# Kernel optimization log

Hardware: AMD Instinct MI355X
Metric: run time of the kernel (lower is better)

## Reference

```python
import jax, jax.numpy as jnp
import numpy as np

DIM = 1024
B, L = 8, 2048
ACT = DIM // 4          # sparse_ratio 0.25
HID = DIM // 4          # LowRankFF reduction 4
EPS = 1e-6
K, DILATION = 5, 1
PAD = (K - 1) * DILATION // 2


def setup_inputs() -> dict:
    key = jax.random.key(0)
    ks = jax.random.split(key, 16)
    s = lambda fan_in: 1.0 / np.sqrt(fan_in)
    return {
        "x": jax.random.normal(ks[0], (B, L, DIM), jnp.float32),
        "norm_w": jnp.ones((DIM,), jnp.float32),
        "dw_w": jax.random.normal(ks[1], (DIM, 1, K), jnp.float32) * s(K),
        "dw_b": jax.random.normal(ks[2], (DIM,), jnp.float32) * s(K),
        "pw_w": jax.random.normal(ks[3], (DIM, DIM), jnp.float32) * s(DIM),
        "pw_b": jax.random.normal(ks[4], (DIM,), jnp.float32) * s(DIM),
        "alpha": jnp.full((ACT,), 0.9, jnp.float32),
        "beta": jnp.full((ACT,), 0.1, jnp.float32),
        "W1_w": jax.random.normal(ks[5], (DIM, DIM), jnp.float32) * s(DIM),
        "W1_b": jax.random.normal(ks[6], (DIM,), jnp.float32) * s(DIM),
        "W2_w": jax.random.normal(ks[7], (DIM, DIM), jnp.float32) * s(DIM),
        "W2_b": jax.random.normal(ks[8], (DIM,), jnp.float32) * s(DIM),
        "down_w": jax.random.normal(ks[9], (HID, DIM), jnp.float32) * s(DIM),
        "down_b": jax.random.normal(ks[10], (HID,), jnp.float32) * s(DIM),
        "up_w": jax.random.normal(ks[11], (DIM, HID), jnp.float32) * s(HID),
        "up_b": jax.random.normal(ks[12], (DIM,), jnpp := jnp.float32) * s(HID),
    }


def reference(x, norm_w, dw_w, dw_b, pw_w, pw_b, alpha, beta,
              W1_w, W1_b, W2_w, W2_b, down_w, down_b, up_w, up_b):
    residual = x
    # RMSNorm
    rms = jnp.sqrt(jnp.mean(x * x, axis=-1, keepdims=True) + EPS)
    xn = norm_w * (x / rms)                              # [B,L,D]
    # depthwise conv (groups=DIM), NCH layout; same-length output
    xc = jax.lax.conv_general_dilated(
        xn.transpose(0, 2, 1), dw_w,
        window_strides=(1,), padding=[(PAD, PAD)],
        rhs_dilation=(DILATION,), feature_group_count=DIM,
        dimension_numbers=("NCH", "OIH", "NCH")) + dw_b[None, :, None]
    xc = xc.transpose(0, 2, 1)                           # [B,L,D]
    # pointwise conv == dense linear over channels
    x_conv = jnp.einsum("bld,od->blo", xc, pw_w) + pw_b
    # sparse shift-gate recurrence on FIRST ACT channels (faithful to source)
    x_act = xn[:, :, :ACT]                               # [B,L,A]

    def step(h, xt):                                     # h,xt: [B,A]
        h = alpha * h + beta * xt
        return h, h

    _, hs = jax.lax.scan(step, jnp.zeros((B, ACT), xn.dtype),
                         x_act.transpose(1, 0, 2))       # hs: [L,B,A]
    x_rec = jnp.concatenate([hs.transpose(1, 0, 2), xn[:, :, ACT:]], axis=-1)
    # gated fusion
    y = x_conv + x_rec
    y = y + jax.nn.sigmoid(y @ W1_w.T + W1_b) * jnp.tanh(y @ W2_w.T + W2_b)
    # low-rank FF (exact gelu, matching torch F.gelu default)
    y = y + (jax.nn.gelu(y @ down_w.T + down_b, approximate=False) @ up_w.T + up_b)
    return y + residual
```

## Files before the change

kernel.cpp:

```cpp
#include <hip/hip_runtime.h>
#include <math.h>

#define DIMC 1024
#define BB   8
#define LL   2048
#define ACTC 256
#define HIDC 256
#define EPSV 1e-6f
#define MROWS (BB * LL)
#define NCHUNK 32
#define LC     64

typedef __bf16 bf16x8 __attribute__((ext_vector_type(8)));
typedef float  f32x4  __attribute__((ext_vector_type(4)));

__device__ __forceinline__ unsigned short f2bf(float f) {
    union { float f; unsigned int u; } v; v.f = f;
    unsigned int u = v.u + 0x7fffu + ((v.u >> 16) & 1u);
    return (unsigned short)(u >> 16);
}
__device__ __forceinline__ float bf2f(unsigned short s) {
    union { float f; unsigned int u; } v; v.u = ((unsigned int)s) << 16;
    return v.f;
}
__device__ __forceinline__ float fast_sigmoid(float x) {
    return 1.0f / (1.0f + __expf(-x));
}
__device__ __forceinline__ float fast_tanh(float x) {
    float ax = fabsf(x);
    float t = 1.0f - 2.0f / (__expf(2.0f * ax) + 1.0f);
    return copysignf(t, x);
}

__global__ void k_convert5(const float* __restrict__ s0, const float* __restrict__ s1,
                           const float* __restrict__ s2, const float* __restrict__ s3,
                           const float* __restrict__ s4,
                           unsigned short* __restrict__ d0, unsigned short* __restrict__ d12,
                           unsigned short* __restrict__ d3, unsigned short* __restrict__ d4) {
    int i = blockIdx.x * blockDim.x + threadIdx.x;
    if (i < 1048576) {
        d0[i] = f2bf(s0[i]);
    } else if (i < 2097152) {
        int j = i - 1048576; int n = j >> 10, kk = j & 1023;
        d12[(size_t)(n * 2) * 1024 + kk] = f2bf(s1[j]);
    } else if (i < 3145728) {
        int j = i - 2097152; int n = j >> 10, kk = j & 1023;
        d12[(size_t)(n * 2 + 1) * 1024 + kk] = f2bf(s2[j]);
    } else if (i < 3407872) {
        d3[i - 3145728] = f2bf(s3[i - 3145728]);
    } else if (i < 3670016) {
        d4[i - 3407872] = f2bf(s4[i - 3407872]);
    }
}

__global__ __launch_bounds__(256, 2) void k_normconv(
        const float* __restrict__ x, const float* __restrict__ w,
        const float* __restrict__ dww, const float* __restrict__ dwb,
        unsigned short* __restrict__ xnb, unsigned short* __restrict__ xc) {
    __shared__ unsigned short sxn[36 * 1024];
    int blk = blockIdx.x;
    int b = blk >> 6, s = blk & 63;
    int l0 = s * 32;
    int t = threadIdx.x;
    int lane = t & 63, wid = t >> 6;

    float4 nw[4];
#pragma unroll
    for (int j = 0; j < 4; ++j) nw[j] = ((const float4*)w)[j * 64 + lane];

    for (int rr = wid; rr < 36; rr += 4) {
        int l = l0 - 2 + rr;
        bool inr = (l >= 0 && l < LL);
        float4 v[4];
#pragma unroll
        for (int j = 0; j < 4; ++j) { v[j].x = 0.f; v[j].y = 0.f; v[j].z = 0.f; v[j].w = 0.f; }
        if (inr) {
            const float4* xp = (const float4*)(x + ((size_t)b * LL + l) * DIMC);
#pragma unroll
            for (int j = 0; j < 4; ++j) v[j] = xp[j * 64 + lane];
        }
        float ss = 0.f;
#pragma unroll
        for (int j = 0; j < 4; ++j)
            ss += v[j].x * v[j].x + v[j].y * v[j].y + v[j].z * v[j].z + v[j].w * v[j].w;
#pragma unroll
        for (int off = 1; off < 64; off <<= 1) ss += __shfl_xor(ss, off, 64);
        float rinv = 1.0f / sqrtf(ss * (1.0f / DIMC) + EPSV);
#pragma unroll
        for (int j = 0; j < 4; ++j) {
            uint2 o;
            o.x = (unsigned)f2bf(nw[j].x * v[j].x * rinv) | ((unsigned)f2bf(nw[j].y * v[j].y * rinv) << 16);
            o.y = (unsigned)f2bf(nw[j].z * v[j].z * rinv) | ((unsigned)f2bf(nw[j].w * v[j].w * rinv) << 16);
            ((uint2*)(sxn + rr * 1024))[j * 64 + lane] = o;
            if (inr && rr >= 2 && rr < 34)
                ((uint2*)(xnb + ((size_t)b * LL + l) * DIMC))[j * 64 + lane] = o;
        }
    }
    __syncthreads();

    float wgt[4][5];
    int c0 = t * 4;
#pragma unroll
    for (int j = 0; j < 4; ++j)
#pragma unroll
        for (int k = 0; k < 5; ++k) wgt[j][k] = dww[(c0 + j) * 5 + k];
    float4 bv = ((const float4*)dwb)[t];
    for (int r = 0; r < 32; ++r) {
        float acc[4] = {bv.x, bv.y, bv.z, bv.w};
#pragma unroll
        for (int k = 0; k < 5; ++k) {
            uint2 rv = ((const uint2*)(sxn + (r + k) * 1024))[t];
            acc[0] += bf2f((unsigned short)(rv.x & 0xffff)) * wgt[0][k];
            acc[1] += bf2f((unsigned short)(rv.x >> 16))    * wgt[1][k];
            acc[2] += bf2f((unsigned short)(rv.y & 0xffff)) * wgt[2][k];
            acc[3] += bf2f((unsigned short)(rv.y >> 16))    * wgt[3][k];
        }
        uint2 o;
        o.x = (unsigned)f2bf(acc[0]) | ((unsigned)f2bf(acc[1]) << 16);
        o.y = (unsigned)f2bf(acc[2]) | ((unsigned)f2bf(acc[3]) << 16);
        ((uint2*)(xc + ((size_t)b * LL + l0 + r) * DIMC))[t] = o;
    }
}

__global__ __launch_bounds__(256) void k_scan_a(const unsigned short* __restrict__ xnb,
                                                const float* __restrict__ alpha,
                                                const float* __restrict__ beta,
                                                float* __restrict__ F) {
    int blk = blockIdx.x;
    int b = blk >> 5, k = blk & (NCHUNK - 1);
    int c = threadIdx.x;
    float a = alpha[c], bt = beta[c];
    const unsigned short* p = xnb + ((size_t)(b * LL + k * LC)) * DIMC + c;
    float h = 0.0f;
    for (int l = 0; l < LC; ++l) h = a * h + bt * bf2f(p[(size_t)l * DIMC]);
    F[(size_t)blk * ACTC + c] = h;
}
__global__ __launch_bounds__(256) void k_scan_c(const unsigned short* __restrict__ xnb,
                                                const float* __restrict__ alpha,
                                                const float* __restrict__ beta,
                                                const float* __restrict__ F,
                                                unsigned short* __restrict__ hs) {
    int blk = blockIdx.x;
    int b = blk >> 5, k = blk & (NCHUNK - 1);
    int c = threadIdx.x;
    float a = alpha[c], bt = beta[c];
    float aL = a;
#pragma unroll
    for (int i = 0; i < 6; ++i) aL *= aL;
    float T = 0.0f;
    for (int j = 0; j < k; ++j)
        T = F[((size_t)b * NCHUNK + j) * ACTC + c] + aL * T;
    const unsigned short* p = xnb + ((size_t)(b * LL + k * LC)) * DIMC + c;
    unsigned short*       q = hs  + ((size_t)(b * LL + k * LC)) * ACTC + c;
    float h = T;
    for (int l = 0; l < LC; ++l) {
        h = a * h + bt * bf2f(p[(size_t)l * DIMC]);
        q[(size_t)l * ACTC] = f2bf(h);
    }
}

#define TM 128
#define TN 128
#define BK 64

#define GLOAD_LDS(gp, lp) \
    __builtin_amdgcn_global_load_lds((const __attribute__((address_space(1))) unsigned int*)(gp), \
                                     (__attribute__((address_space(3))) unsigned int*)(lp), 16, 0, 0)

template<int MODE>
__global__ __launch_bounds__(256, 4) void k_gemm(
        const unsigned short* __restrict__ A,
        const unsigned short* __restrict__ B0,
        const float* __restrict__ bias0,
        const float* __restrict__ bias1,
        const unsigned short* __restrict__ add0,
        const unsigned short* __restrict__ add1,
        const float* __restrict__ addf,
        float* __restrict__ outf,
        unsigned short* __restrict__ outb,
        int M, int N, int K)
{
    __shared__ __align__(16) char lds[32768];
    unsigned short* sA  = (unsigned short*)lds;
    unsigned short* sB0 = (unsigned short*)(lds + 16384);

    int nx = gridDim.x;
    int bid = blockIdx.y * nx + blockIdx.x;
    int xcd = bid & 7, s = bid >> 3;
    int colt = s % nx, rowgrp = s / nx;
    int m0 = (rowgrp * 8 + xcd) * TM;
    int n0 = colt * TN;

    int t = threadIdx.x;
    int w = t >> 6, lane = t & 63;
    int wm = (w >> 1) * 64, wn = (w & 1) * 64;
    int quad = lane >> 4, lm = lane & 15;
    int lm7 = lm & 7;

    f32x4 zero = {0.f, 0.f, 0.f, 0.f};
    f32x4 acc0[4][4];
#pragma unroll
    for (int i = 0; i < 4; ++i)
#pragma unroll
        for (int j = 0; j < 4; ++j) acc0[i][j] = zero;

    for (int k0 = 0; k0 < K; k0 += BK) {
        __syncthreads();
#pragma unroll
        for (int c = 0; c < 4; ++c) {
            int i = t + c * 256;
            int r = i >> 3;
            int sc = ((i & 7) ^ (r & 7)) << 3;
            GLOAD_LDS(A  + (size_t)(m0 + r) * K + k0 + sc, sA  + i * 8);
            GLOAD_LDS(B0 + (size_t)(n0 + r) * K + k0 + sc, sB0 + i * 8);
        }
        __syncthreads();

#pragma unroll
        for (int ks = 0; ks < BK; ks += 32) {
            int cgb = ks >> 3;
            bf16x8 af[4], b0f[4];
#pragma unroll
            for (int i = 0; i < 4; ++i) {
                int sg = ((cgb + quad) ^ lm7) << 3;
                af[i]  = *(const bf16x8*)(sA  + (wm + i * 16 + lm) * BK + sg);
                b0f[i] = *(const bf16x8*)(sB0 + (wn + i * 16 + lm) * BK + sg);
            }
#pragma unroll
            for (int mi = 0; mi < 4; ++mi)
#pragma unroll
                for (int ni = 0; ni < 4; ++ni)
                    acc0[mi][ni] = __builtin_amdgcn_mfma_f32_16x16x32_bf16(af[mi], b0f[ni], acc0[mi][ni], 0, 0, 0);
        }
    }

    __syncthreads();
    if constexpr (MODE == 3) {
        float* sO = (float*)lds;
#pragma unroll
        for (int half = 0; half < 2; ++half) {
            if (wm == half * 64) {
#pragma unroll
                for (int mi = 0; mi < 4; ++mi) {
#pragma unroll
                    for (int ni = 0; ni < 4; ++ni) {
                        int nl = wn + ni * 16 + lm;
                        float bn = bias0[n0 + nl];
#pragma unroll
                        for (int j = 0; j < 4; ++j) {
                            int mloc = mi * 16 + quad * 4 + j;
                            sO[mloc * TN + nl] = acc0[mi][ni][j] + bn;
                        }
                    }
                }
            }
            __syncthreads();
#pragma unroll
            for (int c = 0; c < 8; ++c) {
                int i = t + c * 256;
                int r = i >> 5, c4 = (i & 31) << 2;
                int m = m0 + half * 64 + r, n = n0 + c4;
                float4 v  = *(float4*)(sO + r * TN + c4);
                uint2  ab = *(const uint2*)(add0 + (size_t)m * N + n);
                float4 xf = *(const float4*)(addf + (size_t)m * N + n);
                float4 o;
                o.x = v.x + bf2f((unsigned short)(ab.x & 0xffff)) + xf.x;
                o.y = v.y + bf2f((unsigned short)(ab.x >> 16))    + xf.y;
                o.z = v.z + bf2f((unsigned short)(ab.y & 0xffff)) + xf.z;
                o.w = v.w + bf2f((unsigned short)(ab.y >> 16))    + xf.w;
                *(float4*)(outf + (size_t)m * N + n) = o;
            }
            __syncthreads();
        }
    } else if constexpr (MODE == 4) {
        unsigned short* sO = (unsigned short*)lds;
#pragma unroll
        for (int mi = 0; mi < 4; ++mi) {
#pragma unroll
            for (int ni = 0; ni < 4; ++ni) {
                int nl = wn + ni * 16 + lm;
                int ng = n0 + nl;
                float bn = (nl & 1) ? bias1[ng >> 1] : bias0[ng >> 1];
#pragma unroll
                for (int j = 0; j < 4; ++j) {
                    int ml = wm + mi * 16 + quad * 4 + j;
                    float u  = acc0[mi][ni][j] + bn;
                    float uo = __shfl_xor(u, 1, 64);
                    float ue = (nl & 1) ? uo : u;
                    float ut = (nl & 1) ? u  : uo;
                    float r = fast_sigmoid(ue) * fast_tanh(ut);
                    if (!(nl & 1)) sO[ml * 64 + (nl >> 1)] = f2bf(r);
                }
            }
        }
        __syncthreads();
#pragma unroll
        for (int c = 0; c < 4; ++c) {
            int i = t + c * 256;
            int r = i >> 3, c8 = (i & 7) << 3;
            int m = m0 + r, n = (n0 >> 1) + c8;
            uint4 g  = *(uint4*)(sO + r * 64 + c8);
            uint4 av = *(const uint4*)(add0 + (size_t)m * DIMC + n);
            unsigned* gp = (unsigned*)&g;
            unsigned* ap = (unsigned*)&av;
            uint4 o; unsigned* op = (unsigned*)&o;
#pragma unroll
            for (int q = 0; q < 4; ++q) {
                float lo = bf2f((unsigned short)(gp[q] & 0xffff)) + bf2f((unsigned short)(ap[q] & 0xffff));
                float hi = bf2f((unsigned short)(gp[q] >> 16))    + bf2f((unsigned short)(ap[q] >> 16));
                op[q] = (unsigned)f2bf(lo) | ((unsigned)f2bf(hi) << 16);
            }
            *(uint4*)(outb + (size_t)m * DIMC + n) = o;
        }
    } else {
        unsigned short* sO = (unsigned short*)lds;
#pragma unroll
        for (int mi = 0; mi < 4; ++mi) {
#pragma unroll
            for (int ni = 0; ni < 4; ++ni) {
                int nl = wn + ni * 16 + lm;
                int n  = n0 + nl;
                float bn = bias0[n];
#pragma unroll
                for (int j = 0; j < 4; ++j) {
                    int ml = wm + mi * 16 + quad * 4 + j;
                    float v = acc0[mi][ni][j];
                    float r;
                    if constexpr (MODE == 0) {
                        r = v + bn;
                    } else {
                        float u = v + bn;
                        r = 0.5f * u * (1.0f + erff(u * 0.70710678118654752f));
                    }
                    sO[ml * TN + nl] = f2bf(r);
                }
            }
        }
        __syncthreads();
#pragma unroll
        for (int c = 0; c < 8; ++c) {
            int i = t + c * 256;
            int r = i >> 4, c8 = (i & 15) << 3;
            int m = m0 + r, n = n0 + c8;
            uint4 g = *(uint4*)(sO + r * TN + c8);
            if constexpr (MODE == 2) {
                *(uint4*)(outb + (size_t)m * N + n) = g;
            } else {
                uint4 av = (n0 < ACTC) ? *(const uint4*)(add0 + (size_t)m * ACTC + n)
                                       : *(const uint4*)(add1 + (size_t)m * DIMC + n);
                unsigned* gp = (unsigned*)&g;
                unsigned* ap = (unsigned*)&av;
                uint4 o;
                unsigned* op = (unsigned*)&o;
#pragma unroll
                for (int q = 0; q < 4; ++q) {
                    float lo = bf2f((unsigned short)(gp[q] & 0xffff)) + bf2f((unsigned short)(ap[q] & 0xffff));
                    float hi = bf2f((unsigned short)(gp[q] >> 16))    + bf2f((unsigned short)(ap[q] >> 16));
                    op[q] = (unsigned)f2bf(lo) | ((unsigned)f2bf(hi) << 16);
                }
                *(uint4*)(outb + (size_t)m * N + n) = o;
            }
        }
    }
}

template<int MODE>
__global__ __launch_bounds__(256, 4) void k_gemm64(
        const unsigned short* __restrict__ A,
        const unsigned short* __restrict__ B0,
        const float* __restrict__ bias0,
        unsigned short* __restrict__ outb,
        int M, int N, int K)
{
    __shared__ __align__(16) char lds[24576];
    unsigned short* sA  = (unsigned short*)lds;
    unsigned short* sB0 = (unsigned short*)(lds + 16384);

    int nx = gridDim.x;
    int bid = blockIdx.y * nx + blockIdx.x;
    int xcd = bid & 7, s = bid >> 3;
    int colt = s % nx, rowgrp = s / nx;
    int m0 = (rowgrp * 8 + xcd) * TM;
    int n0 = colt * 64;

    int t = threadIdx.x;
    int w = t >> 6, lane = t & 63;
    int wm = (w >> 1) * 64, wn = (w & 1) * 32;
    int quad = lane >> 4, lm = lane & 15;
    int lm7 = lm & 7;

    f32x4 zero = {0.f, 0.f, 0.f, 0.f};
    f32x4 acc0[4][2];
#pragma unroll
    for (int i = 0; i < 4; ++i)
#pragma unroll
        for (int j = 0; j < 2; ++j) acc0[i][j] = zero;

    for (int k0 = 0; k0 < K; k0 += BK) {
        __syncthreads();
#pragma unroll
        for (int c = 0; c < 4; ++c) {
            int i = t + c * 256;
            int r = i >> 3;
            int sc = ((i & 7) ^ (r & 7)) << 3;
            GLOAD_LDS(A + (size_t)(m0 + r) * K + k0 + sc, sA + i * 8);
        }
#pragma unroll
        for (int c = 0; c < 2; ++c) {
            int i = t + c * 256;
            int r = i >> 3;
            int sc = ((i & 7) ^ (r & 7)) << 3;
            GLOAD_LDS(B0 + (size_t)(n0 + r) * K + k0 + sc, sB0 + i * 8);
        }
        __syncthreads();

#pragma unroll
        for (int ks = 0; ks < BK; ks += 32) {
            int cgb = ks >> 3;
            int sg = ((cgb + quad) ^ lm7) << 3;
            bf16x8 af[4], b0f[2];
#pragma unroll
            for (int i = 0; i < 4; ++i)
                af[i] = *(const bf16x8*)(sA + (wm + i * 16 + lm) * BK + sg);
#pragma unroll
            for (int i = 0; i < 2; ++i)
                b0f[i] = *(const bf16x8*)(sB0 + (wn + i * 16 + lm) * BK + sg);
#pragma unroll
            for (int mi = 0; mi < 4; ++mi)
#pragma unroll
                for (int ni = 0; ni < 2; ++ni)
                    acc0[mi][ni] = __builtin_amdgcn_mfma_f32_16x16x32_bf16(af[mi], b0f[ni], acc0[mi][ni], 0, 0, 0);
        }
    }

    __syncthreads();
    unsigned short* sO = (unsigned short*)lds;
#pragma unroll
    for (int mi = 0; mi < 4; ++mi) {
#pragma unroll
        for (int ni = 0; ni < 2; ++ni) {
            int nl = wn + ni * 16 + lm;
            int n  = n0 + nl;
            float bn = bias0[n];
#pragma unroll
            for (int j = 0; j < 4; ++j) {
                int ml = wm + mi * 16 + quad * 4 + j;
                float u = acc0[mi][ni][j] + bn;
                float r = 0.5f * u * (1.0f + erff(u * 0.70710678118654752f));
                sO[ml * 64 + nl] = f2bf(r);
            }
        }
    }
    __syncthreads();
#pragma unroll
    for (int c = 0; c < 4; ++c) {
        int i = t + c * 256;
        int r = i >> 3, c8 = (i & 7) << 3;
        int m = m0 + r, n = n0 + c8;
        uint4 g = *(uint4*)(sO + r * 64 + c8);
        *(uint4*)(outb + (size_t)m * N + n) = g;
    }
}

extern "C" void kernel_launch(void* const* d_in, const int* in_sizes, int n_in,
                              void* d_out, int out_size, void* d_ws, size_t ws_size,
                              hipStream_t stream) {
    (void)in_sizes; (void)n_in; (void)out_size; (void)ws_size;
    const float* x      = (const float*)d_in[0];
    const float* norm_w = (const float*)d_in[1];
    const float* dw_w   = (const float*)d_in[2];
    const float* dw_b   = (const float*)d_in[3];
    const float* pw_w   = (const float*)d_in[4];
    const float* pw_b   = (const float*)d_in[5];
    const float* alpha  = (const float*)d_in[6];
    const float* beta   = (const float*)d_in[7];
    const float* W1_w   = (const float*)d_in[8];
    const float* W1_b   = (const float*)d_in[9];
    const float* W2_w   = (const float*)d_in[10];
    const float* W2_b   = (const float*)d_in[11];
    const float* down_w = (const float*)d_in[12];
    const float* down_b = (const float*)d_in[13];
    const float* up_w   = (const float*)d_in[14];
    const float* up_b   = (const float*)d_in[15];

    char* ws = (char*)d_ws;
    unsigned short* xnb  = (unsigned short*)(ws);
    unsigned short* xc   = (unsigned short*)(ws + 33554432ull);
    unsigned short* hs   = (unsigned short*)(ws + 67108864ull);
    unsigned short* y1b  = (unsigned short*)(ws + 75497472ull);
    unsigned short* y2b  = (unsigned short*)(ws + 109051904ull);
    unsigned short* gact = (unsigned short*)(ws + 142606336ull);
    unsigned short* wpw  = (unsigned short*)(ws + 150994944ull);
    unsigned short* w12  = wpw + 1048576;
    unsigned short* wdn  = wpw + 3145728;
    unsigned short* wup  = wdn + 262144;
    float*          Fb   = (float*)(ws + 159383552ull);

    k_convert5<<<14336, 256, 0, stream>>>(pw_w, W1_w, W2_w, down_w, up_w,
                                          wpw, w12, wdn, wup);

    k_normconv<<<BB * 64, 256, 0, stream>>>(x, norm_w, dw_w, dw_b, xnb, xc);

    k_scan_a<<<BB * NCHUNK, ACTC, 0, stream>>>(xnb, alpha, beta, Fb);
    k_scan_c<<<BB * NCHUNK, ACTC, 0, stream>>>(xnb, alpha, beta, Fb, hs);

    dim3 g0(DIMC / TN, MROWS / TM);
    dim3 g1(2 * DIMC / TN, MROWS / TM);
    dim3 g2(HIDC / 64, MROWS / TM);
    k_gemm<0><<<g0, 256, 0, stream>>>(xc, wpw, pw_b, nullptr, hs, xnb, nullptr, nullptr, y1b, MROWS, DIMC, DIMC);
    k_gemm<4><<<g1, 256, 0, stream>>>(y1b, w12, W1_b, W2_b, y1b, nullptr, nullptr, nullptr, y2b, MROWS, 2 * DIMC, DIMC);
    k_gemm64<2><<<g2, 256, 0, stream>>>(y2b, wdn, down_b, gact, MROWS, HIDC, DIMC);
    k_gemm<3><<<g0, 256, 0, stream>>>(gact, wup, up_b, nullptr, y2b, nullptr, x, (float*)d_out, nullptr, MROWS, DIMC, HIDC);
}
```

Measured before the change: 372.6 us.

## Compute W1 and W2 GEMMs in one kernel with dual accumulators sharing A tile

Replaces the interleaved 2048-wide W1/W2 GEMM, which paired sigmoid and tanh columns via lane shuffles, with a dual-B GEMM. Each block loads one A tile and two B tiles and keeps two accumulator sets, then applies sigmoid*tanh directly in the epilogue. This halves the number of A-tile loads and removes the shuffle and the interleaved weight layout. The cost is more registers and LDS per block, so occupancy drops to 2 waves per SIMD.

```diff
diff --git a/kernel.cpp b/kernel.cpp
--- a/kernel.cpp
+++ b/kernel.cpp
@@ -35,22 +35,15 @@
 __global__ void k_convert5(const float* __restrict__ s0, const float* __restrict__ s1,
                            const float* __restrict__ s2, const float* __restrict__ s3,
                            const float* __restrict__ s4,
-                           unsigned short* __restrict__ d0, unsigned short* __restrict__ d12,
-                           unsigned short* __restrict__ d3, unsigned short* __restrict__ d4) {
+                           unsigned short* __restrict__ d0, unsigned short* __restrict__ d1,
+                           unsigned short* __restrict__ d2, unsigned short* __restrict__ d3,
+                           unsigned short* __restrict__ d4) {
     int i = blockIdx.x * blockDim.x + threadIdx.x;
-    if (i < 1048576) {
-        d0[i] = f2bf(s0[i]);
-    } else if (i < 2097152) {
-        int j = i - 1048576; int n = j >> 10, kk = j & 1023;
-        d12[(size_t)(n * 2) * 1024 + kk] = f2bf(s1[j]);
-    } else if (i < 3145728) {
-        int j = i - 2097152; int n = j >> 10, kk = j & 1023;
-        d12[(size_t)(n * 2 + 1) * 1024 + kk] = f2bf(s2[j]);
-    } else if (i < 3407872) {
-        d3[i - 3145728] = f2bf(s3[i - 3145728]);
-    } else if (i < 3670016) {
-        d4[i - 3407872] = f2bf(s4[i - 3407872]);
-    }
+    if (i < 1048576)            d0[i]           = f2bf(s0[i]);
+    else if (i < 2097152)       d1[i - 1048576] = f2bf(s1[i - 1048576]);
+    else if (i < 3145728)       d2[i - 2097152] = f2bf(s2[i - 2097152]);
+    else if (i < 3407872)       d3[i - 3145728] = f2bf(s3[i - 3145728]);
+    else if (i < 3670016)       d4[i - 3407872] = f2bf(s4[i - 3407872]);
 }
 
 __global__ __launch_bounds__(256, 2) void k_normconv(
@@ -168,9 +161,10 @@
                                      (__attribute__((address_space(3))) unsigned int*)(lp), 16, 0, 0)
 
 template<int MODE>
-__global__ __launch_bounds__(256, 4) void k_gemm(
+__device__ __forceinline__ void gemm_body(
         const unsigned short* __restrict__ A,
         const unsigned short* __restrict__ B0,
+        const unsigned short* __restrict__ B1,
         const float* __restrict__ bias0,
         const float* __restrict__ bias1,
         const unsigned short* __restrict__ add0,
@@ -180,9 +174,11 @@
         unsigned short* __restrict__ outb,
         int M, int N, int K)
 {
-    __shared__ __align__(16) char lds[32768];
+    constexpr int LDSB = (MODE == 1) ? 49152 : 32768;
+    __shared__ __align__(16) char lds[LDSB];
     unsigned short* sA  = (unsigned short*)lds;
     unsigned short* sB0 = (unsigned short*)(lds + 16384);
+    unsigned short* sB1 = (unsigned short*)(lds + 32768);
 
     int nx = gridDim.x;
     int bid = blockIdx.y * nx + blockIdx.x;
@@ -199,10 +195,17 @@
 
     f32x4 zero = {0.f, 0.f, 0.f, 0.f};
     f32x4 acc0[4][4];
+    f32x4 acc1[(MODE == 1) ? 4 : 1][(MODE == 1) ? 4 : 1];
 #pragma unroll
     for (int i = 0; i < 4; ++i)
 #pragma unroll
         for (int j = 0; j < 4; ++j) acc0[i][j] = zero;
+    if constexpr (MODE == 1) {
+#pragma unroll
+        for (int i = 0; i < 4; ++i)
+#pragma unroll
+            for (int j = 0; j < 4; ++j) acc1[i][j] = zero;
+    }
 
     for (int k0 = 0; k0 < K; k0 += BK) {
         __syncthreads();
@@ -213,6 +216,8 @@
             int sc = ((i & 7) ^ (r & 7)) << 3;
             GLOAD_LDS(A  + (size_t)(m0 + r) * K + k0 + sc, sA  + i * 8);
             GLOAD_LDS(B0 + (size_t)(n0 + r) * K + k0 + sc, sB0 + i * 8);
+            if constexpr (MODE == 1)
+                GLOAD_LDS(B1 + (size_t)(n0 + r) * K + k0 + sc, sB1 + i * 8);
         }
         __syncthreads();
 
@@ -226,11 +231,25 @@
                 af[i]  = *(const bf16x8*)(sA  + (wm + i * 16 + lm) * BK + sg);
                 b0f[i] = *(const bf16x8*)(sB0 + (wn + i * 16 + lm) * BK + sg);
             }
-#pragma unroll
-            for (int mi = 0; mi < 4; ++mi)
-#pragma unroll
-                for (int ni = 0; ni < 4; ++ni)
-                    acc0[mi][ni] = __builtin_amdgcn_mfma_f32_16x16x32_bf16(af[mi], b0f[ni], acc0[mi][ni], 0, 0, 0);
+            if constexpr (MODE == 1) {
+                bf16x8 b1f[4];
+#pragma unroll
+                for (int i = 0; i < 4; ++i)
+                    b1f[i] = *(const bf16x8*)(sB1 + (wn + i * 16 + lm) * BK + (((cgb + quad) ^ lm7) << 3));
+#pragma unroll
+                for (int mi = 0; mi < 4; ++mi)
+#pragma unroll
+                    for (int ni = 0; ni < 4; ++ni) {
+                        acc0[mi][ni] = __builtin_amdgcn_mfma_f32_16x16x32_bf16(af[mi], b0f[ni], acc0[mi][ni], 0, 0, 0);
+                        acc1[mi][ni] = __builtin_amdgcn_mfma_f32_16x16x32_bf16(af[mi], b1f[ni], acc1[mi][ni], 0, 0, 0);
+                    }
+            } else {
+#pragma unroll
+                for (int mi = 0; mi < 4; ++mi)
+#pragma unroll
+                    for (int ni = 0; ni < 4; ++ni)
+                        acc0[mi][ni] = __builtin_amdgcn_mfma_f32_16x16x32_bf16(af[mi], b0f[ni], acc0[mi][ni], 0, 0, 0);
+            }
         }
     }
 
@@ -272,46 +291,6 @@
             }
             __syncthreads();
         }
-    } else if constexpr (MODE == 4) {
-        unsigned short* sO = (unsigned short*)lds;
-#pragma unroll
-        for (int mi = 0; mi < 4; ++mi) {
-#pragma unroll
-            for (int ni = 0; ni < 4; ++ni) {
-                int nl = wn + ni * 16 + lm;
-                int ng = n0 + nl;
-                float bn = (nl & 1) ? bias1[ng >> 1] : bias0[ng >> 1];
-#pragma unroll
-                for (int j = 0; j < 4; ++j) {
-                    int ml = wm + mi * 16 + quad * 4 + j;
-                    float u  = acc0[mi][ni][j] + bn;
-                    float uo = __shfl_xor(u, 1, 64);
-                    float ue = (nl & 1) ? uo : u;
-                    float ut = (nl & 1) ? u  : uo;
-                    float r = fast_sigmoid(ue) * fast_tanh(ut);
-                    if (!(nl & 1)) sO[ml * 64 + (nl >> 1)] = f2bf(r);
-                }
-            }
-        }
-        __syncthreads();
-#pragma unroll
-        for (int c = 0; c < 4; ++c) {
-            int i = t + c * 256;
-            int r = i >> 3, c8 = (i & 7) << 3;
-            int m = m0 + r, n = (n0 >> 1) + c8;
-            uint4 g  = *(uint4*)(sO + r * 64 + c8);
-            uint4 av = *(const uint4*)(add0 + (size_t)m * DIMC + n);
-            unsigned* gp = (unsigned*)&g;
-            unsigned* ap = (unsigned*)&av;
-            uint4 o; unsigned* op = (unsigned*)&o;
-#pragma unroll
-            for (int q = 0; q < 4; ++q) {
-                float lo = bf2f((unsigned short)(gp[q] & 0xffff)) + bf2f((unsigned short)(ap[q] & 0xffff));
-                float hi = bf2f((unsigned short)(gp[q] >> 16))    + bf2f((unsigned short)(ap[q] >> 16));
-                op[q] = (unsigned)f2bf(lo) | ((unsigned)f2bf(hi) << 16);
-            }
-            *(uint4*)(outb + (size_t)m * DIMC + n) = o;
-        }
     } else {
         unsigned short* sO = (unsigned short*)lds;
 #pragma unroll
@@ -321,6 +300,7 @@
                 int nl = wn + ni * 16 + lm;
                 int n  = n0 + nl;
                 float bn = bias0[n];
+                float bn1 = (MODE == 1) ? bias1[n] : 0.0f;
 #pragma unroll
                 for (int j = 0; j < 4; ++j) {
                     int ml = wm + mi * 16 + quad * 4 + j;
@@ -329,8 +309,9 @@
                     if constexpr (MODE == 0) {
                         r = v + bn;
                     } else {
-                        float u = v + bn;
-                        r = 0.5f * u * (1.0f + erff(u * 0.70710678118654752f));
+                        float u1 = v + bn;
+                        float u2 = acc1[mi][ni][j] + bn1;
+                        r = fast_sigmoid(u1) * fast_tanh(u2);
                     }
                     sO[ml * TN + nl] = f2bf(r);
                 }
@@ -343,29 +324,48 @@
             int r = i >> 4, c8 = (i & 15) << 3;
             int m = m0 + r, n = n0 + c8;
             uint4 g = *(uint4*)(sO + r * TN + c8);
-            if constexpr (MODE == 2) {
-                *(uint4*)(outb + (size_t)m * N + n) = g;
+            uint4 av;
+            if constexpr (MODE == 0) {
+                av = (n0 < ACTC) ? *(const uint4*)(add0 + (size_t)m * ACTC + n)
+                                 : *(const uint4*)(add1 + (size_t)m * DIMC + n);
             } else {
-                uint4 av = (n0 < ACTC) ? *(const uint4*)(add0 + (size_t)m * ACTC + n)
-                                       : *(const uint4*)(add1 + (size_t)m * DIMC + n);
-                unsigned* gp = (unsigned*)&g;
-                unsigned* ap = (unsigned*)&av;
-                uint4 o;
-                unsigned* op = (unsigned*)&o;
-#pragma unroll
-                for (int q = 0; q < 4; ++q) {
-                    float lo = bf2f((unsigned short)(gp[q] & 0xffff)) + bf2f((unsigned short)(ap[q] & 0xffff));
-                    float hi = bf2f((unsigned short)(gp[q] >> 16))    + bf2f((unsigned short)(ap[q] >> 16));
-                    op[q] = (unsigned)f2bf(lo) | ((unsigned)f2bf(hi) << 16);
-                }
-                *(uint4*)(outb + (size_t)m * N + n) = o;
-            }
-        }
-    }
-}
-
-template<int MODE>
-__global__ __launch_bounds__(256, 4) void k_gemm64(
+                av = *(const uint4*)(add0 + (size_t)m * N + n);
+            }
+            unsigned* gp = (unsigned*)&g;
+            unsigned* ap = (unsigned*)&av;
+            uint4 o;
+            unsigned* op = (unsigned*)&o;
+#pragma unroll
+            for (int q = 0; q < 4; ++q) {
+                float lo = bf2f((unsigned short)(gp[q] & 0xffff)) + bf2f((unsigned short)(ap[q] & 0xffff));
+                float hi = bf2f((unsigned short)(gp[q] >> 16))    + bf2f((unsigned short)(ap[q] >> 16));
+                op[q] = (unsigned)f2bf(lo) | ((unsigned)f2bf(hi) << 16);
+            }
+            *(uint4*)(outb + (size_t)m * N + n) = o;
+        }
+    }
+}
+
+__global__ __launch_bounds__(256, 4) void k_gemm_pw(
+        const unsigned short* A, const unsigned short* B0, const float* bias0,
+        const unsigned short* add0, const unsigned short* add1, unsigned short* outb,
+        int M, int N, int K) {
+    gemm_body<0>(A, B0, nullptr, bias0, nullptr, add0, add1, nullptr, nullptr, outb, M, N, K);
+}
+__global__ __launch_bounds__(256, 2) void k_gemm_glu(
+        const unsigned short* A, const unsigned short* B0, const unsigned short* B1,
+        const float* bias0, const float* bias1, const unsigned short* add0,
+        unsigned short* outb, int M, int N, int K) {
+    gemm_body<1>(A, B0, B1, bias0, bias1, add0, nullptr, nullptr, nullptr, outb, M, N, K);
+}
+__global__ __launch_bounds__(256, 4) void k_gemm_up(
+        const unsigned short* A, const unsigned short* B0, const float* bias0,
+        const unsigned short* add0, const float* addf, float* outf,
+        int M, int N, int K) {
+    gemm_body<3>(A, B0, nullptr, bias0, nullptr, add0, nullptr, addf, outf, nullptr, M, N, K);
+}
+
+__global__ __launch_bounds__(256, 4) void k_gemm_dn(
         const unsigned short* __restrict__ A,
         const unsigned short* __restrict__ B0,
         const float* __restrict__ bias0,
@@ -491,13 +491,14 @@
     unsigned short* y2b  = (unsigned short*)(ws + 109051904ull);
     unsigned short* gact = (unsigned short*)(ws + 142606336ull);
     unsigned short* wpw  = (unsigned short*)(ws + 150994944ull);
-    unsigned short* w12  = wpw + 1048576;
-    unsigned short* wdn  = wpw + 3145728;
+    unsigned short* w1b  = wpw + 1048576;
+    unsigned short* w2b  = w1b + 1048576;
+    unsigned short* wdn  = w2b + 1048576;
     unsigned short* wup  = wdn + 262144;
     float*          Fb   = (float*)(ws + 159383552ull);
 
     k_convert5<<<14336, 256, 0, stream>>>(pw_w, W1_w, W2_w, down_w, up_w,
-                                          wpw, w12, wdn, wup);
+                                          wpw, w1b, w2b, wdn, wup);
 
     k_normconv<<<BB * 64, 256, 0, stream>>>(x, norm_w, dw_w, dw_b, xnb, xc);
 
@@ -505,10 +506,9 @@
     k_scan_c<<<BB * NCHUNK, ACTC, 0, stream>>>(xnb, alpha, beta, Fb, hs);
 
     dim3 g0(DIMC / TN, MROWS / TM);
-    dim3 g1(2 * DIMC / TN, MROWS / TM);
     dim3 g2(HIDC / 64, MROWS / TM);
-    k_gemm<0><<<g0, 256, 0, stream>>>(xc, wpw, pw_b, nullptr, hs, xnb, nullptr, nullptr, y1b, MROWS, DIMC, DIMC);
-    k_gemm<4><<<g1, 256, 0, stream>>>(y1b, w12, W1_b, W2_b, y1b, nullptr, nullptr, nullptr, y2b, MROWS, 2 * DIMC, DIMC);
-    k_gemm64<2><<<g2, 256, 0, stream>>>(y2b, wdn, down_b, gact, MROWS, HIDC, DIMC);
-    k_gemm<3><<<g0, 256, 0, stream>>>(gact, wup, up_b, nullptr, y2b, nullptr, x, (float*)d_out, nullptr, MROWS, DIMC, HIDC);
-}
+    k_gemm_pw <<<g0, 256, 0, stream>>>(xc, wpw, pw_b, hs, xnb, y1b, MROWS, DIMC, DIMC);
+    k_gemm_glu<<<g0, 256, 0, stream>>>(y1b, w1b, w2b, W1_b, W2_b, y1b, y2b, MROWS, DIMC, DIMC);
+    k_gemm_dn <<<g2, 256, 0, stream>>>(y2b, wdn, down_b, gact, MROWS, HIDC, DIMC);
+    k_gemm_up <<<g0, 256, 0, stream>>>(gact, wup, up_b, y2b, x, (float*)d_out, MROWS, DIMC, HIDC);
+}
```

After: 349.5 us. -6.2%, faster.
